# Performance work log

Measured on AMD Instinct MI355X. Metric: run time of the kernel, lower is better.

Reference implementation:

```python
import jax, jax.numpy as jnp
import numpy as np

HEADS = 16
DIM_HEAD = 64

def setup_inputs() -> dict:
    key = jax.random.key(0)
    ks = jax.random.split(key, 5)
    B, S, D = 2, 2048, 1024
    return {
        "hidden_states": jax.random.normal(ks[0], (B, S, D), dtype=jnp.float32),
        "Wq": jax.random.normal(ks[1], (D, D), dtype=jnp.float32) * (D ** -0.5),
        "Wkv": jax.random.normal(ks[2], (D, D), dtype=jnp.float32) * (D ** -0.5),
        "Wout": jax.random.normal(ks[3], (D, D), dtype=jnp.float32) * (D ** -0.5),
        "bout": jnp.zeros((D,), dtype=jnp.float32),
    }

def reference(hidden_states, Wq, Wkv, Wout, bout):
    B, S, D = hidden_states.shape
    H, Dh = HEADS, DIM_HEAD
    # projections (torch Linear: x @ W.T; here weights are stored as [in, out])
    q = hidden_states @ Wq            # [B, S, D]
    kv = hidden_states @ Wkv          # key == value share the to_kv projection
    q = q.reshape(B, S, H, Dh).transpose(0, 2, 1, 3)   # [B, H, S, Dh]
    k = kv.reshape(B, S, H, Dh).transpose(0, 2, 1, 3)
    v = k
    scale = 1.0 / np.sqrt(Dh).astype(np.float32)
    # ReLU attention: no softmax
    attn = jax.nn.relu(jnp.einsum("bhsd,bhtd->bhst", q, k) * scale)  # [B,H,S,S]
    out = jnp.einsum("bhst,bhtd->bhsd", attn, v)                     # [B,H,S,Dh]
    out = out.transpose(0, 2, 1, 3).reshape(B, S, H * Dh)
    return out @ Wout + bout
```

## Files before the change

kernel.cpp:

```cpp
#include <hip/hip_runtime.h>
#include <hip/hip_bf16.h>

#define HEADS  16
#define DIMH   64
#define NBATCH 2
#define SEQ    2048
#define DMODEL 1024
#define MROWS  (NBATCH * SEQ)

typedef __attribute__((ext_vector_type(8)))  short bf16x8;
typedef __attribute__((ext_vector_type(4)))  float f32x4;
typedef __attribute__((ext_vector_type(16))) float f32x16;
typedef __attribute__((ext_vector_type(4)))  float float4v;
typedef __attribute__((ext_vector_type(4)))  short short4v;

__device__ inline void glds16(const void* g, void* l) {
    __builtin_amdgcn_global_load_lds(
        (const __attribute__((address_space(1))) unsigned int*)g,
        (__attribute__((address_space(3))) unsigned int*)l, 16, 0, 0);
}

#define WAIT_VMCNT(N) asm volatile("s_waitcnt vmcnt(" #N ")" ::: "memory")
#define BARRIER() do { __builtin_amdgcn_s_barrier(); asm volatile("" ::: "memory"); } while (0)

__global__ void cvt_kernel(const float* __restrict__ in,
                           __hip_bfloat16* __restrict__ out, int n4) {
    int i = blockIdx.x * blockDim.x + threadIdx.x;
    if (i >= n4) return;
    float4v v = reinterpret_cast<const float4v*>(in)[i];
    union { short4v s; __hip_bfloat16 h[4]; } u;
#pragma unroll
    for (int j = 0; j < 4; ++j) u.h[j] = __float2bfloat16(v[j]);
    reinterpret_cast<short4v*>(out)[i] = u.s;
}

__global__ void tr_kernel(const float* __restrict__ W,
                          __hip_bfloat16* __restrict__ WT) {
    __shared__ float tile[32][33];
    int i = blockIdx.y * 32 + threadIdx.y;
    int o = blockIdx.x * 32 + threadIdx.x;
    tile[threadIdx.y][threadIdx.x] = W[i * DMODEL + o];
    __syncthreads();
    int oo = blockIdx.x * 32 + threadIdx.y;
    int ii = blockIdx.y * 32 + threadIdx.x;
    WT[oo * DMODEL + ii] = __float2bfloat16(tile[threadIdx.x][threadIdx.y]);
}


__launch_bounds__(512, 2)
__global__ void proj_kernel(const __hip_bfloat16* __restrict__ hsb,
                            const __hip_bfloat16* __restrict__ WqT,
                            const __hip_bfloat16* __restrict__ WkvT,
                            __hip_bfloat16* __restrict__ qb,
                            __hip_bfloat16* __restrict__ kb,
                            __hip_bfloat16* __restrict__ vtb) {
    __shared__ __align__(16) char SLDS[73728];
    char (*Alds)[8192]  = (char (*)[8192])SLDS;
    char (*Blds)[16384] = (char (*)[16384])(SLDS + 24576);
    char* CT = SLDS;

    const int tid  = threadIdx.x;
    const int wave = tid >> 6;
    const int lane = tid & 63;
    const int lr = lane & 15;
    const int lk = lane >> 4;
    const int wm = wave >> 2, wn = wave & 3;

    int bid = blockIdx.x;
    bid = (bid & 7) * 32 + (bid >> 3);
    const int xt = bid & 7;
    const int mt = bid >> 3;
    const bool is_q = xt < 4;
    const int mbase = mt * 128;
    const int nbase = (xt & 3) * 256;
    const __hip_bfloat16* __restrict__ WT = is_q ? WqT : WkvT;

    const char* __restrict__ Ab = (const char*)(hsb + (size_t)mbase * DMODEL);
    const char* __restrict__ Bb = (const char*)(WT + (size_t)nbase * DMODEL);

    auto stage = [&](int buf, int k0) {
        const size_t colb = (size_t)k0 * 2 + lk * 16;
        glds16(Ab + (size_t)(wave * 16 + lr) * (DMODEL * 2) + colb,
               &Alds[buf][wave * 1024]);
#pragma unroll
        for (int r = 0; r < 2; ++r)
            glds16(Bb + (size_t)((r * 8 + wave) * 16 + lr) * (DMODEL * 2) + colb,
                   &Blds[buf][r * 8192 + wave * 1024]);
    };

    stage(0, 0);
    stage(1, 32);

    f32x4 acc[4][4] = {};
    int c0 = 0;
    for (int t = 0; t < DMODEL / 32; ++t) {
        if (t < DMODEL / 32 - 1) WAIT_VMCNT(3); else WAIT_VMCNT(0);
        BARRIER();
        if (t + 2 < DMODEL / 32) {
            int sb = c0 + 2; if (sb >= 3) sb -= 3;
            stage(sb, (t + 2) * 32);
        }
        bf16x8 af[4], bfr[4];
#pragma unroll
        for (int i = 0; i < 4; ++i) {
            af[i]  = *reinterpret_cast<const bf16x8*>(&Alds[c0][(wm * 4 + i) * 1024 + lane * 16]);
            bfr[i] = *reinterpret_cast<const bf16x8*>(&Blds[c0][(wn * 4 + i) * 1024 + lane * 16]);
        }
#pragma unroll
        for (int i = 0; i < 4; ++i)
#pragma unroll
            for (int j = 0; j < 4; ++j)
                acc[i][j] = __builtin_amdgcn_mfma_f32_16x16x32_bf16(af[i], bfr[j], acc[i][j], 0, 0, 0);
        c0 = (c0 + 1 == 3) ? 0 : c0 + 1;
    }

    const float qscale = is_q ? 0.125f : 1.0f;
    const int b_ = mbase >> 11;
    const int s0 = mbase & (SEQ - 1);
    BARRIER();

#pragma unroll
    for (int i = 0; i < 4; ++i)
#pragma unroll
        for (int j = 0; j < 4; ++j)
#pragma unroll
            for (int r = 0; r < 4; ++r) {
                int m = wm * 64 + i * 16 + lk * 4 + r;
                int n = wn * 64 + j * 16 + lr;
                *reinterpret_cast<__hip_bfloat16*>(
                    &CT[m * 512 + ((n * 2) ^ (((m >> 2) & 7) << 4))]) =
                    __float2bfloat16(acc[i][j][r] * qscale);
            }
    BARRIER();

    __hip_bfloat16* __restrict__ dst0 = is_q ? qb : kb;
#pragma unroll
    for (int p = 0; p < 8; ++p) {
        int g = p * 64 + (tid >> 3);
        int m = g >> 2, seg = g & 3, o = tid & 7;
        int key = ((m >> 2) & 7) << 4;
        bf16x8 val = *reinterpret_cast<const bf16x8*>(
            &CT[m * 512 + ((seg * 128 + o * 16) ^ key)]);
        int h = (nbase >> 6) + seg;
        *reinterpret_cast<bf16x8*>(
            &dst0[(((size_t)b_ * HEADS + h) * SEQ + s0 + m) * DIMH + o * 8]) = val;
    }

    if (!is_q) {
        BARRIER();
#pragma unroll
        for (int i = 0; i < 4; ++i)
#pragma unroll
            for (int j = 0; j < 4; ++j)
#pragma unroll
                for (int r = 0; r < 4; ++r) {
                    int m = wm * 64 + i * 16 + lk * 4 + r;
                    int n = wn * 64 + j * 16 + lr;
                    *reinterpret_cast<__hip_bfloat16*>(
                        &CT[n * 256 + ((m * 2) ^ ((n & 7) << 4))]) =
                        __float2bfloat16(acc[i][j][r]);
                }
        BARRIER();
#pragma unroll
        for (int p = 0; p < 8; ++p) {
            int g = p * 64 + (tid >> 3);
            int n = g >> 1, half = g & 1, o = tid & 7;
            int key2 = (n & 7) << 4;
            int D = half * 64 + o * 8;
            int mm = D >> 4, H = o & 1;
            union { unsigned long long d[2]; bf16x8 v; } val;
            val.d[0] = *reinterpret_cast<const unsigned long long*>(
                &CT[n * 256 + ((mm * 32 + H * 8) ^ key2)]);
            val.d[1] = *reinterpret_cast<const unsigned long long*>(
                &CT[n * 256 + ((mm * 32 + 16 + H * 8) ^ key2)]);
            int h = (nbase >> 6) + (n >> 6);
            int dh = n & 63;
            *reinterpret_cast<bf16x8*>(
                &vtb[(((size_t)b_ * HEADS + h) * DIMH + dh) * SEQ + s0 + D]) = val.v;
        }
    }
}

__launch_bounds__(512, 2)
__global__ void outproj_kernel(const __hip_bfloat16* __restrict__ ao,
                               const __hip_bfloat16* __restrict__ WoT,
                               const float* __restrict__ bout,
                               float* __restrict__ out) {
    __shared__ __align__(16) char Alds[3][8192];
    __shared__ __align__(16) char Blds[3][8192];
    const int tid  = threadIdx.x;
    const int wave = tid >> 6;
    const int lane = tid & 63;
    const int lr = lane & 15;
    const int lk = lane >> 4;
    const int wm = wave >> 1, wn = wave & 1;

    int bid = blockIdx.x;
    bid = (bid & 7) * 32 + (bid >> 3);
    const int xt = bid & 7;
    const int mt = bid >> 3;
    const int mbase = mt * 128;
    const int nbase = xt * 128;

    const char* __restrict__ Ab = (const char*)(ao + (size_t)mbase * DMODEL);
    const char* __restrict__ Bb = (const char*)(WoT + (size_t)nbase * DMODEL);

    auto stage = [&](int buf, int k0) {
        const size_t colb = (size_t)k0 * 2 + lk * 16;
        glds16(Ab + (size_t)(wave * 16 + lr) * (DMODEL * 2) + colb,
               &Alds[buf][wave * 1024]);
        glds16(Bb + (size_t)(wave * 16 + lr) * (DMODEL * 2) + colb,
               &Blds[buf][wave * 1024]);
    };

    stage(0, 0);
    stage(1, 32);

    f32x4 acc[2][4] = {};
    int c0 = 0;
    for (int t = 0; t < DMODEL / 32; ++t) {
        if (t < DMODEL / 32 - 1) WAIT_VMCNT(2); else WAIT_VMCNT(0);
        BARRIER();
        if (t + 2 < DMODEL / 32) {
            int sb = c0 + 2; if (sb >= 3) sb -= 3;
            stage(sb, (t + 2) * 32);
        }
        bf16x8 af[2], bfr[4];
#pragma unroll
        for (int i = 0; i < 2; ++i)
            af[i] = *reinterpret_cast<const bf16x8*>(&Alds[c0][(wm * 2 + i) * 1024 + lane * 16]);
#pragma unroll
        for (int j = 0; j < 4; ++j)
            bfr[j] = *reinterpret_cast<const bf16x8*>(&Blds[c0][(wn * 4 + j) * 1024 + lane * 16]);
#pragma unroll
        for (int i = 0; i < 2; ++i)
#pragma unroll
            for (int j = 0; j < 4; ++j)
                acc[i][j] = __builtin_amdgcn_mfma_f32_16x16x32_bf16(af[i], bfr[j], acc[i][j], 0, 0, 0);
        c0 = (c0 + 1 == 3) ? 0 : c0 + 1;
    }

#pragma unroll
    for (int j = 0; j < 4; ++j) {
        const int n = nbase + wn * 64 + j * 16 + lr;
        const float bias = bout[n];
#pragma unroll
        for (int i = 0; i < 2; ++i) {
#pragma unroll
            for (int r = 0; r < 4; ++r) {
                int m = mbase + wm * 32 + i * 16 + lk * 4 + r;
                out[(size_t)m * DMODEL + n] = acc[i][j][r] + bias;
            }
        }
    }
}

__launch_bounds__(256, 2)
__global__ void attn_kernel(const __hip_bfloat16* __restrict__ qb,
                            const __hip_bfloat16* __restrict__ kb,
                            const __hip_bfloat16* __restrict__ vtb,
                            __hip_bfloat16* __restrict__ ao) {
    __shared__ __align__(16) char Klds[4][8192];
    __shared__ __align__(16) char Vlds[4][8192];
    const int lane = threadIdx.x & 63;
    const int wave = threadIdx.x >> 6;
    const int l32  = lane & 31;
    const int hi   = lane >> 5;

    int bid = blockIdx.x;
    bid = (bid & 7) * 64 + (bid >> 3);
    const int bh   = bid >> 4;
    const int qblk = bid & 15;
    const int b_ = bh >> 4, h = bh & 15;
    const int qbase = qblk * 128 + wave * 32;

    const __hip_bfloat16* __restrict__ Q = qb + (size_t)bh * SEQ * DIMH;
    const char* __restrict__ Kg = (const char*)(kb  + (size_t)bh * SEQ * DIMH);
    const char* __restrict__ Vg = (const char*)(vtb + (size_t)bh * DIMH * SEQ);

    bf16x8 qf[4];
#pragma unroll
    for (int ks = 0; ks < 4; ++ks)
        qf[ks] = *reinterpret_cast<const bf16x8*>(
            &Q[(size_t)(qbase + l32) * DIMH + ks * 16 + hi * 8]);

    auto stage = [&](int buf, int t0) {
#pragma unroll
        for (int p = 0; p < 2; ++p) {
            glds16(Kg + (size_t)(t0 + p * 32 + (lane & 31)) * 128 +
                       wave * 32 + (lane >> 5) * 16,
                   &Klds[buf][(p * 4 + wave) * 1024]);
            const int rv = p * 4 + wave;
            glds16(Vg + (size_t)((rv & 1) * 32 + (lane & 31)) * (SEQ * 2) +
                       (size_t)(t0 + (rv >> 1) * 16) * 2 + (lane >> 5) * 16,
                   &Vlds[buf][rv * 1024]);
        }
    };

    f32x16 acco[2] = {};
    f32x16 sp0, sp1;

    auto do_qk = [&](const char* Kc) {
        sp0 = f32x16{}; sp1 = f32x16{};
        __builtin_amdgcn_s_setprio(1);
#pragma unroll
        for (int ks = 0; ks < 4; ++ks) {
            bf16x8 k0f = *reinterpret_cast<const bf16x8*>(Kc + ks * 1024 + lane * 16);
            bf16x8 k1f = *reinterpret_cast<const bf16x8*>(Kc + (4 + ks) * 1024 + lane * 16);
            sp0 = __builtin_amdgcn_mfma_f32_32x32x16_bf16(k0f, qf[ks], sp0, 0, 0, 0);
            sp1 = __builtin_amdgcn_mfma_f32_32x32x16_bf16(k1f, qf[ks], sp1, 0, 0, 0);
        }
        __builtin_amdgcn_s_setprio(0);
    };

    auto do_packpv = [&](const char* Vc) {
        __builtin_amdgcn_s_setprio(1);
#pragma unroll
        for (int kt = 0; kt < 4; ++kt) {
            union { __hip_bfloat16 hh[8]; bf16x8 v; } pa;
            const int rb = (kt & 1) * 8;
#pragma unroll
            for (int j = 0; j < 8; ++j) {
                float x = (kt < 2) ? sp0[rb + j] : sp1[rb + j];
                pa.hh[j] = __float2bfloat16(fmaxf(x, 0.f));
            }
#pragma unroll
            for (int nt = 0; nt < 2; ++nt) {
                bf16x8 vbv = *reinterpret_cast<const bf16x8*>(
                    Vc + (kt * 2 + nt) * 1024 + lane * 16);
                acco[nt] = __builtin_amdgcn_mfma_f32_32x32x16_bf16(pa.v, vbv, acco[nt], 0, 0, 0);
            }
        }
        __builtin_amdgcn_s_setprio(0);
    };

    stage(0, 0);
    stage(1, 64);

    WAIT_VMCNT(4);
    BARRIER();
    stage(2, 128);
    do_qk(Klds[0]);

    for (int t = 1; t < SEQ / 64; ++t) {
        if (t < SEQ / 64 - 1) WAIT_VMCNT(4); else WAIT_VMCNT(0);
        BARRIER();
        if (t + 2 < SEQ / 64) stage((t + 2) & 3, (t + 2) * 64);
        do_packpv(Vlds[(t - 1) & 3]);
        do_qk(Klds[t & 3]);
    }
    do_packpv(Vlds[(SEQ / 64 - 1) & 3]);

#pragma unroll
    for (int nt = 0; nt < 2; ++nt) {
#pragma unroll
        for (int r = 0; r < 16; ++r) {
            int q = qbase + (r & 3) + 8 * (r >> 2) + 4 * hi;
            ao[(size_t)(b_ * SEQ + q) * DMODEL + h * 64 + nt * 32 + l32] =
                __float2bfloat16(acco[nt][r]);
        }
    }
}

extern "C" void kernel_launch(void* const* d_in, const int* in_sizes, int n_in,
                              void* d_out, int out_size, void* d_ws, size_t ws_size,
                              hipStream_t stream) {
    const float* hs   = (const float*)d_in[0];
    const float* Wq   = (const float*)d_in[1];
    const float* Wkv  = (const float*)d_in[2];
    const float* Wout = (const float*)d_in[3];
    const float* bout = (const float*)d_in[4];
    float* out = (float*)d_out;

    char* ws = (char*)d_ws;
    size_t off = 0;
    auto alloc = [&](size_t bytes) { char* p = ws + off; off += bytes; return p; };
    __hip_bfloat16* hsb  = (__hip_bfloat16*)alloc((size_t)MROWS * DMODEL * 2);
    __hip_bfloat16* WqT  = (__hip_bfloat16*)alloc((size_t)DMODEL * DMODEL * 2);
    __hip_bfloat16* WkvT = (__hip_bfloat16*)alloc((size_t)DMODEL * DMODEL * 2);
    __hip_bfloat16* WoT  = (__hip_bfloat16*)alloc((size_t)DMODEL * DMODEL * 2);
    __hip_bfloat16* qb   = (__hip_bfloat16*)alloc((size_t)MROWS * DMODEL * 2);
    __hip_bfloat16* kb   = (__hip_bfloat16*)alloc((size_t)MROWS * DMODEL * 2);
    __hip_bfloat16* vtb  = (__hip_bfloat16*)alloc((size_t)MROWS * DMODEL * 2);
    __hip_bfloat16* ao   = hsb;

    cvt_kernel<<<(MROWS * DMODEL / 4 + 255) / 256, 256, 0, stream>>>(hs, hsb, MROWS * DMODEL / 4);
    dim3 trg(32, 32), trb(32, 32);
    tr_kernel<<<trg, trb, 0, stream>>>(Wq, WqT);
    tr_kernel<<<trg, trb, 0, stream>>>(Wkv, WkvT);
    tr_kernel<<<trg, trb, 0, stream>>>(Wout, WoT);

    proj_kernel<<<256, 512, 0, stream>>>(hsb, WqT, WkvT, qb, kb, vtb);

    attn_kernel<<<NBATCH * HEADS * (SEQ / 128), 256, 0, stream>>>(qb, kb, vtb, ao);

    outproj_kernel<<<256, 512, 0, stream>>>(ao, WoT, bout, out);
}
```

Before: 120.6 us.

## Split attention over key range with 512-thread blocks and combine partials

The attention kernel now uses 512-thread blocks covering 256 queries each, and splits the key sequence into two halves handled by separate blocks. Each block writes fp32 partial outputs to a workspace, and a new combine kernel sums the two partials and converts them to bf16 for the output projection. Bigger blocks halve the K/V staging traffic per query, and the key split keeps the same block count of 512. The cost is an extra kernel launch plus writing and re-reading two fp32 partial tensors of about 16 MB each.

```diff
diff --git a/kernel.cpp b/kernel.cpp
--- a/kernel.cpp
+++ b/kernel.cpp
@@ -31,6 +31,19 @@
     union { short4v s; __hip_bfloat16 h[4]; } u;
 #pragma unroll
     for (int j = 0; j < 4; ++j) u.h[j] = __float2bfloat16(v[j]);
+    reinterpret_cast<short4v*>(out)[i] = u.s;
+}
+
+__global__ void combine_kernel(const float* __restrict__ p0,
+                               const float* __restrict__ p1,
+                               __hip_bfloat16* __restrict__ out, int n4) {
+    int i = blockIdx.x * blockDim.x + threadIdx.x;
+    if (i >= n4) return;
+    float4v a = reinterpret_cast<const float4v*>(p0)[i];
+    float4v b = reinterpret_cast<const float4v*>(p1)[i];
+    union { short4v s; __hip_bfloat16 h[4]; } u;
+#pragma unroll
+    for (int j = 0; j < 4; ++j) u.h[j] = __float2bfloat16(a[j] + b[j]);
     reinterpret_cast<short4v*>(out)[i] = u.s;
 }
 
@@ -255,11 +268,11 @@
     }
 }
 
-__launch_bounds__(256, 2)
+__launch_bounds__(512, 2)
 __global__ void attn_kernel(const __hip_bfloat16* __restrict__ qb,
                             const __hip_bfloat16* __restrict__ kb,
                             const __hip_bfloat16* __restrict__ vtb,
-                            __hip_bfloat16* __restrict__ ao) {
+                            float* __restrict__ po) {
     __shared__ __align__(16) char Klds[4][8192];
     __shared__ __align__(16) char Vlds[4][8192];
     const int lane = threadIdx.x & 63;
@@ -269,10 +282,12 @@
 
     int bid = blockIdx.x;
     bid = (bid & 7) * 64 + (bid >> 3);
+    const int ts   = bid & 1;
+    const int qblk = (bid >> 1) & 7;
     const int bh   = bid >> 4;
-    const int qblk = bid & 15;
     const int b_ = bh >> 4, h = bh & 15;
-    const int qbase = qblk * 128 + wave * 32;
+    const int qbase = qblk * 256 + wave * 32;
+    const int tbeg = ts * (SEQ / 2);
 
     const __hip_bfloat16* __restrict__ Q = qb + (size_t)bh * SEQ * DIMH;
     const char* __restrict__ Kg = (const char*)(kb  + (size_t)bh * SEQ * DIMH);
@@ -285,16 +300,12 @@
             &Q[(size_t)(qbase + l32) * DIMH + ks * 16 + hi * 8]);
 
     auto stage = [&](int buf, int t0) {
-#pragma unroll
-        for (int p = 0; p < 2; ++p) {
-            glds16(Kg + (size_t)(t0 + p * 32 + (lane & 31)) * 128 +
-                       wave * 32 + (lane >> 5) * 16,
-                   &Klds[buf][(p * 4 + wave) * 1024]);
-            const int rv = p * 4 + wave;
-            glds16(Vg + (size_t)((rv & 1) * 32 + (lane & 31)) * (SEQ * 2) +
-                       (size_t)(t0 + (rv >> 1) * 16) * 2 + (lane >> 5) * 16,
-                   &Vlds[buf][rv * 1024]);
-        }
+        glds16(Kg + (size_t)(t0 + (wave >> 2) * 32 + (lane & 31)) * 128 +
+                   (wave & 3) * 32 + (lane >> 5) * 16,
+               &Klds[buf][wave * 1024]);
+        glds16(Vg + (size_t)((wave & 1) * 32 + (lane & 31)) * (SEQ * 2) +
+                   (size_t)(t0 + (wave >> 1) * 16) * 2 + (lane >> 5) * 16,
+               &Vlds[buf][wave * 1024]);
     };
 
     f32x16 acco[2] = {};
@@ -334,30 +345,31 @@
         __builtin_amdgcn_s_setprio(0);
     };
 
-    stage(0, 0);
-    stage(1, 64);
-
-    WAIT_VMCNT(4);
+    const int NT = SEQ / 2 / 64;
+    stage(0, tbeg);
+    stage(1, tbeg + 64);
+
+    WAIT_VMCNT(2);
     BARRIER();
-    stage(2, 128);
+    stage(2, tbeg + 128);
     do_qk(Klds[0]);
 
-    for (int t = 1; t < SEQ / 64; ++t) {
-        if (t < SEQ / 64 - 1) WAIT_VMCNT(4); else WAIT_VMCNT(0);
+    for (int t = 1; t < NT; ++t) {
+        if (t < NT - 1) WAIT_VMCNT(2); else WAIT_VMCNT(0);
         BARRIER();
-        if (t + 2 < SEQ / 64) stage((t + 2) & 3, (t + 2) * 64);
+        if (t + 2 < NT) stage((t + 2) & 3, tbeg + (t + 2) * 64);
         do_packpv(Vlds[(t - 1) & 3]);
         do_qk(Klds[t & 3]);
     }
-    do_packpv(Vlds[(SEQ / 64 - 1) & 3]);
-
+    do_packpv(Vlds[(NT - 1) & 3]);
+
+    float* __restrict__ PO = po + (size_t)ts * MROWS * DMODEL;
 #pragma unroll
     for (int nt = 0; nt < 2; ++nt) {
 #pragma unroll
         for (int r = 0; r < 16; ++r) {
             int q = qbase + (r & 3) + 8 * (r >> 2) + 4 * hi;
-            ao[(size_t)(b_ * SEQ + q) * DMODEL + h * 64 + nt * 32 + l32] =
-                __float2bfloat16(acco[nt][r]);
+            PO[(size_t)(b_ * SEQ + q) * DMODEL + h * 64 + nt * 32 + l32] = acco[nt][r];
         }
     }
 }
@@ -382,6 +394,7 @@
     __hip_bfloat16* qb   = (__hip_bfloat16*)alloc((size_t)MROWS * DMODEL * 2);
     __hip_bfloat16* kb   = (__hip_bfloat16*)alloc((size_t)MROWS * DMODEL * 2);
     __hip_bfloat16* vtb  = (__hip_bfloat16*)alloc((size_t)MROWS * DMODEL * 2);
+    float*          po   = (float*)alloc((size_t)2 * MROWS * DMODEL * 4);
     __hip_bfloat16* ao   = hsb;
 
     cvt_kernel<<<(MROWS * DMODEL / 4 + 255) / 256, 256, 0, stream>>>(hs, hsb, MROWS * DMODEL / 4);
@@ -392,7 +405,10 @@
 
     proj_kernel<<<256, 512, 0, stream>>>(hsb, WqT, WkvT, qb, kb, vtb);
 
-    attn_kernel<<<NBATCH * HEADS * (SEQ / 128), 256, 0, stream>>>(qb, kb, vtb, ao);
+    attn_kernel<<<512, 512, 0, stream>>>(qb, kb, vtb, po);
+
+    combine_kernel<<<(MROWS * DMODEL / 4 + 255) / 256, 256, 0, stream>>>(
+        po, po + (size_t)MROWS * DMODEL, ao, MROWS * DMODEL / 4);
 
     outproj_kernel<<<256, 512, 0, stream>>>(ao, WoT, bout, out);
 }
```

Measured after the change: 120.9 us. About the same (+0.2%).

## Replace LDS-staged attention with single-wave blocks loading K/V directly to registers

Applied to the files above, without the earlier changes.

The attention kernel drops the shared-memory K/V ring buffer and its barriers. Each 64-thread block now handles 32 queries and loads K and V fragments straight from global memory into registers, double-buffered across two register sets. This removes LDS traffic and block-wide synchronisation, but K/V reuse across waves now depends on L2/L1 instead of shared memory, and register pressure rises.

```diff
diff --git a/kernel.cpp b/kernel.cpp
--- a/kernel.cpp
+++ b/kernel.cpp
@@ -255,24 +255,21 @@
     }
 }
 
-__launch_bounds__(256, 2)
+__launch_bounds__(64, 2)
 __global__ void attn_kernel(const __hip_bfloat16* __restrict__ qb,
                             const __hip_bfloat16* __restrict__ kb,
                             const __hip_bfloat16* __restrict__ vtb,
                             __hip_bfloat16* __restrict__ ao) {
-    __shared__ __align__(16) char Klds[4][8192];
-    __shared__ __align__(16) char Vlds[4][8192];
     const int lane = threadIdx.x & 63;
-    const int wave = threadIdx.x >> 6;
     const int l32  = lane & 31;
     const int hi   = lane >> 5;
 
     int bid = blockIdx.x;
-    bid = (bid & 7) * 64 + (bid >> 3);
-    const int bh   = bid >> 4;
-    const int qblk = bid & 15;
+    bid = (bid & 7) * 256 + (bid >> 3);
+    const int bh = bid >> 6;
+    const int qw = bid & 63;
     const int b_ = bh >> 4, h = bh & 15;
-    const int qbase = qblk * 128 + wave * 32;
+    const int qbase = qw * 32;
 
     const __hip_bfloat16* __restrict__ Q = qb + (size_t)bh * SEQ * DIMH;
     const char* __restrict__ Kg = (const char*)(kb  + (size_t)bh * SEQ * DIMH);
@@ -284,37 +281,31 @@
         qf[ks] = *reinterpret_cast<const bf16x8*>(
             &Q[(size_t)(qbase + l32) * DIMH + ks * 16 + hi * 8]);
 
-    auto stage = [&](int buf, int t0) {
-#pragma unroll
-        for (int p = 0; p < 2; ++p) {
-            glds16(Kg + (size_t)(t0 + p * 32 + (lane & 31)) * 128 +
-                       wave * 32 + (lane >> 5) * 16,
-                   &Klds[buf][(p * 4 + wave) * 1024]);
-            const int rv = p * 4 + wave;
-            glds16(Vg + (size_t)((rv & 1) * 32 + (lane & 31)) * (SEQ * 2) +
-                       (size_t)(t0 + (rv >> 1) * 16) * 2 + (lane >> 5) * 16,
-                   &Vlds[buf][rv * 1024]);
-        }
+    auto LOADKV = [&](bf16x8 (&kf)[8], bf16x8 (&vf)[8], int t0) {
+#pragma unroll
+        for (int rh = 0; rh < 2; ++rh)
+#pragma unroll
+            for (int ks = 0; ks < 4; ++ks)
+                kf[rh * 4 + ks] = *reinterpret_cast<const bf16x8*>(
+                    Kg + (size_t)(t0 + rh * 32 + l32) * 128 + ks * 32 + hi * 16);
+#pragma unroll
+        for (int kt = 0; kt < 4; ++kt)
+#pragma unroll
+            for (int nt = 0; nt < 2; ++nt)
+                vf[kt * 2 + nt] = *reinterpret_cast<const bf16x8*>(
+                    Vg + (size_t)(nt * 32 + l32) * (SEQ * 2) + (size_t)(t0 + kt * 16) * 2 + hi * 16);
     };
 
     f32x16 acco[2] = {};
-    f32x16 sp0, sp1;
-
-    auto do_qk = [&](const char* Kc) {
-        sp0 = f32x16{}; sp1 = f32x16{};
+
+    auto COMPUTE = [&](const bf16x8 (&kf)[8], const bf16x8 (&vf)[8]) {
+        f32x16 sp0 = {}, sp1 = {};
         __builtin_amdgcn_s_setprio(1);
 #pragma unroll
         for (int ks = 0; ks < 4; ++ks) {
-            bf16x8 k0f = *reinterpret_cast<const bf16x8*>(Kc + ks * 1024 + lane * 16);
-            bf16x8 k1f = *reinterpret_cast<const bf16x8*>(Kc + (4 + ks) * 1024 + lane * 16);
-            sp0 = __builtin_amdgcn_mfma_f32_32x32x16_bf16(k0f, qf[ks], sp0, 0, 0, 0);
-            sp1 = __builtin_amdgcn_mfma_f32_32x32x16_bf16(k1f, qf[ks], sp1, 0, 0, 0);
-        }
-        __builtin_amdgcn_s_setprio(0);
-    };
-
-    auto do_packpv = [&](const char* Vc) {
-        __builtin_amdgcn_s_setprio(1);
+            sp0 = __builtin_amdgcn_mfma_f32_32x32x16_bf16(kf[ks], qf[ks], sp0, 0, 0, 0);
+            sp1 = __builtin_amdgcn_mfma_f32_32x32x16_bf16(kf[4 + ks], qf[ks], sp1, 0, 0, 0);
+        }
 #pragma unroll
         for (int kt = 0; kt < 4; ++kt) {
             union { __hip_bfloat16 hh[8]; bf16x8 v; } pa;
@@ -325,31 +316,24 @@
                 pa.hh[j] = __float2bfloat16(fmaxf(x, 0.f));
             }
 #pragma unroll
-            for (int nt = 0; nt < 2; ++nt) {
-                bf16x8 vbv = *reinterpret_cast<const bf16x8*>(
-                    Vc + (kt * 2 + nt) * 1024 + lane * 16);
-                acco[nt] = __builtin_amdgcn_mfma_f32_32x32x16_bf16(pa.v, vbv, acco[nt], 0, 0, 0);
-            }
+            for (int nt = 0; nt < 2; ++nt)
+                acco[nt] = __builtin_amdgcn_mfma_f32_32x32x16_bf16(
+                    pa.v, vf[kt * 2 + nt], acco[nt], 0, 0, 0);
         }
         __builtin_amdgcn_s_setprio(0);
     };
 
-    stage(0, 0);
-    stage(1, 64);
-
-    WAIT_VMCNT(4);
-    BARRIER();
-    stage(2, 128);
-    do_qk(Klds[0]);
-
-    for (int t = 1; t < SEQ / 64; ++t) {
-        if (t < SEQ / 64 - 1) WAIT_VMCNT(4); else WAIT_VMCNT(0);
-        BARRIER();
-        if (t + 2 < SEQ / 64) stage((t + 2) & 3, (t + 2) * 64);
-        do_packpv(Vlds[(t - 1) & 3]);
-        do_qk(Klds[t & 3]);
-    }
-    do_packpv(Vlds[(SEQ / 64 - 1) & 3]);
+    bf16x8 kfA[8], vfA[8], kfB[8], vfB[8];
+    const int NT = SEQ / 64;
+
+    LOADKV(kfA, vfA, 0);
+#pragma unroll 1
+    for (int t = 0; t < NT; t += 2) {
+        LOADKV(kfB, vfB, (t + 1) * 64);
+        COMPUTE(kfA, vfA);
+        if (t + 2 < NT) LOADKV(kfA, vfA, (t + 2) * 64);
+        COMPUTE(kfB, vfB);
+    }
 
 #pragma unroll
     for (int nt = 0; nt < 2; ++nt) {
@@ -392,7 +376,7 @@
 
     proj_kernel<<<256, 512, 0, stream>>>(hsb, WqT, WkvT, qb, kb, vtb);
 
-    attn_kernel<<<NBATCH * HEADS * (SEQ / 128), 256, 0, stream>>>(qb, kb, vtb, ao);
+    attn_kernel<<<2048, 64, 0, stream>>>(qb, kb, vtb, ao);
 
     outproj_kernel<<<256, 512, 0, stream>>>(ao, WoT, bout, out);
 }
```

Measured after the change: 193.1 us. 1.6x slower.

## Retile projection to 128x128 blocks and widen attention blocks to 8 waves

Applied to the files above, without the earlier changes.

The projection GEMM tile shrinks from 128x256 to 128x128. This doubles the grid to 512 blocks, halves LDS use and raises the occupancy hint to 4. The attention kernel moves to 512-thread blocks that each cover 256 queries, so every staged K/V tile is shared by twice as many waves. Its software pipeline, which overlapped QK of one tile with PV of the previous one, is replaced by a simpler fused compute per tile. The aims are better CU fill in the projection and more K/V reuse in attention, at the cost of losing the QK/PV overlap and lowering per-wave reuse in the GEMM.

```diff
diff --git a/kernel.cpp b/kernel.cpp
--- a/kernel.cpp
+++ b/kernel.cpp
@@ -47,16 +47,16 @@
 }
 
 
-__launch_bounds__(512, 2)
+__launch_bounds__(512, 4)
 __global__ void proj_kernel(const __hip_bfloat16* __restrict__ hsb,
                             const __hip_bfloat16* __restrict__ WqT,
                             const __hip_bfloat16* __restrict__ WkvT,
                             __hip_bfloat16* __restrict__ qb,
                             __hip_bfloat16* __restrict__ kb,
                             __hip_bfloat16* __restrict__ vtb) {
-    __shared__ __align__(16) char SLDS[73728];
-    char (*Alds)[8192]  = (char (*)[8192])SLDS;
-    char (*Blds)[16384] = (char (*)[16384])(SLDS + 24576);
+    __shared__ __align__(16) char SLDS[49152];
+    char (*Alds)[8192] = (char (*)[8192])SLDS;
+    char (*Blds)[8192] = (char (*)[8192])(SLDS + 24576);
     char* CT = SLDS;
 
     const int tid  = threadIdx.x;
@@ -64,15 +64,15 @@
     const int lane = tid & 63;
     const int lr = lane & 15;
     const int lk = lane >> 4;
-    const int wm = wave >> 2, wn = wave & 3;
+    const int wm = wave >> 1, wn = wave & 1;
 
     int bid = blockIdx.x;
-    bid = (bid & 7) * 32 + (bid >> 3);
-    const int xt = bid & 7;
-    const int mt = bid >> 3;
-    const bool is_q = xt < 4;
+    bid = (bid & 7) * 64 + (bid >> 3);
+    const int xt = bid & 15;
+    const int mt = bid >> 4;
+    const bool is_q = xt < 8;
     const int mbase = mt * 128;
-    const int nbase = (xt & 3) * 256;
+    const int nbase = (xt & 7) * 128;
     const __hip_bfloat16* __restrict__ WT = is_q ? WqT : WkvT;
 
     const char* __restrict__ Ab = (const char*)(hsb + (size_t)mbase * DMODEL);
@@ -80,34 +80,32 @@
 
     auto stage = [&](int buf, int k0) {
         const size_t colb = (size_t)k0 * 2 + lk * 16;
-        glds16(Ab + (size_t)(wave * 16 + lr) * (DMODEL * 2) + colb,
-               &Alds[buf][wave * 1024]);
-#pragma unroll
-        for (int r = 0; r < 2; ++r)
-            glds16(Bb + (size_t)((r * 8 + wave) * 16 + lr) * (DMODEL * 2) + colb,
-                   &Blds[buf][r * 8192 + wave * 1024]);
+        const size_t rowoff = (size_t)(wave * 16 + lr) * (DMODEL * 2);
+        glds16(Ab + rowoff + colb, &Alds[buf][wave * 1024]);
+        glds16(Bb + rowoff + colb, &Blds[buf][wave * 1024]);
     };
 
     stage(0, 0);
     stage(1, 32);
 
-    f32x4 acc[4][4] = {};
+    f32x4 acc[2][4] = {};
     int c0 = 0;
     for (int t = 0; t < DMODEL / 32; ++t) {
-        if (t < DMODEL / 32 - 1) WAIT_VMCNT(3); else WAIT_VMCNT(0);
+        if (t < DMODEL / 32 - 1) WAIT_VMCNT(2); else WAIT_VMCNT(0);
         BARRIER();
         if (t + 2 < DMODEL / 32) {
             int sb = c0 + 2; if (sb >= 3) sb -= 3;
             stage(sb, (t + 2) * 32);
         }
-        bf16x8 af[4], bfr[4];
-#pragma unroll
-        for (int i = 0; i < 4; ++i) {
-            af[i]  = *reinterpret_cast<const bf16x8*>(&Alds[c0][(wm * 4 + i) * 1024 + lane * 16]);
-            bfr[i] = *reinterpret_cast<const bf16x8*>(&Blds[c0][(wn * 4 + i) * 1024 + lane * 16]);
-        }
-#pragma unroll
-        for (int i = 0; i < 4; ++i)
+        bf16x8 af[2], bfr[4];
+#pragma unroll
+        for (int i = 0; i < 2; ++i)
+            af[i] = *reinterpret_cast<const bf16x8*>(&Alds[c0][(wm * 2 + i) * 1024 + lane * 16]);
+#pragma unroll
+        for (int j = 0; j < 4; ++j)
+            bfr[j] = *reinterpret_cast<const bf16x8*>(&Blds[c0][(wn * 4 + j) * 1024 + lane * 16]);
+#pragma unroll
+        for (int i = 0; i < 2; ++i)
 #pragma unroll
             for (int j = 0; j < 4; ++j)
                 acc[i][j] = __builtin_amdgcn_mfma_f32_16x16x32_bf16(af[i], bfr[j], acc[i][j], 0, 0, 0);
@@ -117,44 +115,44 @@
     const float qscale = is_q ? 0.125f : 1.0f;
     const int b_ = mbase >> 11;
     const int s0 = mbase & (SEQ - 1);
+    const int h0 = nbase >> 6;
     BARRIER();
 
 #pragma unroll
-    for (int i = 0; i < 4; ++i)
+    for (int i = 0; i < 2; ++i)
 #pragma unroll
         for (int j = 0; j < 4; ++j)
 #pragma unroll
             for (int r = 0; r < 4; ++r) {
-                int m = wm * 64 + i * 16 + lk * 4 + r;
+                int m = wm * 32 + i * 16 + lk * 4 + r;
                 int n = wn * 64 + j * 16 + lr;
                 *reinterpret_cast<__hip_bfloat16*>(
-                    &CT[m * 512 + ((n * 2) ^ (((m >> 2) & 7) << 4))]) =
+                    &CT[m * 256 + ((n * 2) ^ (((m >> 2) & 7) << 4))]) =
                     __float2bfloat16(acc[i][j][r] * qscale);
             }
     BARRIER();
 
     __hip_bfloat16* __restrict__ dst0 = is_q ? qb : kb;
 #pragma unroll
-    for (int p = 0; p < 8; ++p) {
+    for (int p = 0; p < 4; ++p) {
         int g = p * 64 + (tid >> 3);
-        int m = g >> 2, seg = g & 3, o = tid & 7;
+        int m = g >> 1, hseg = g & 1, o = tid & 7;
         int key = ((m >> 2) & 7) << 4;
         bf16x8 val = *reinterpret_cast<const bf16x8*>(
-            &CT[m * 512 + ((seg * 128 + o * 16) ^ key)]);
-        int h = (nbase >> 6) + seg;
+            &CT[m * 256 + ((hseg * 128 + o * 16) ^ key)]);
         *reinterpret_cast<bf16x8*>(
-            &dst0[(((size_t)b_ * HEADS + h) * SEQ + s0 + m) * DIMH + o * 8]) = val;
+            &dst0[(((size_t)b_ * HEADS + h0 + hseg) * SEQ + s0 + m) * DIMH + o * 8]) = val;
     }
 
     if (!is_q) {
         BARRIER();
 #pragma unroll
-        for (int i = 0; i < 4; ++i)
+        for (int i = 0; i < 2; ++i)
 #pragma unroll
             for (int j = 0; j < 4; ++j)
 #pragma unroll
                 for (int r = 0; r < 4; ++r) {
-                    int m = wm * 64 + i * 16 + lk * 4 + r;
+                    int m = wm * 32 + i * 16 + lk * 4 + r;
                     int n = wn * 64 + j * 16 + lr;
                     *reinterpret_cast<__hip_bfloat16*>(
                         &CT[n * 256 + ((m * 2) ^ ((n & 7) << 4))]) =
@@ -162,7 +160,7 @@
                 }
         BARRIER();
 #pragma unroll
-        for (int p = 0; p < 8; ++p) {
+        for (int p = 0; p < 4; ++p) {
             int g = p * 64 + (tid >> 3);
             int n = g >> 1, half = g & 1, o = tid & 7;
             int key2 = (n & 7) << 4;
@@ -173,7 +171,7 @@
                 &CT[n * 256 + ((mm * 32 + H * 8) ^ key2)]);
             val.d[1] = *reinterpret_cast<const unsigned long long*>(
                 &CT[n * 256 + ((mm * 32 + 16 + H * 8) ^ key2)]);
-            int h = (nbase >> 6) + (n >> 6);
+            int h = h0 + (n >> 6);
             int dh = n & 63;
             *reinterpret_cast<bf16x8*>(
                 &vtb[(((size_t)b_ * HEADS + h) * DIMH + dh) * SEQ + s0 + D]) = val.v;
@@ -255,7 +253,7 @@
     }
 }
 
-__launch_bounds__(256, 2)
+__launch_bounds__(512, 2)
 __global__ void attn_kernel(const __hip_bfloat16* __restrict__ qb,
                             const __hip_bfloat16* __restrict__ kb,
                             const __hip_bfloat16* __restrict__ vtb,
@@ -268,11 +266,11 @@
     const int hi   = lane >> 5;
 
     int bid = blockIdx.x;
-    bid = (bid & 7) * 64 + (bid >> 3);
-    const int bh   = bid >> 4;
-    const int qblk = bid & 15;
+    bid = (bid & 7) * 32 + (bid >> 3);
+    const int qblk = bid & 7;
+    const int bh   = bid >> 3;
     const int b_ = bh >> 4, h = bh & 15;
-    const int qbase = qblk * 128 + wave * 32;
+    const int qbase = qblk * 256 + wave * 32;
 
     const __hip_bfloat16* __restrict__ Q = qb + (size_t)bh * SEQ * DIMH;
     const char* __restrict__ Kg = (const char*)(kb  + (size_t)bh * SEQ * DIMH);
@@ -285,23 +283,18 @@
             &Q[(size_t)(qbase + l32) * DIMH + ks * 16 + hi * 8]);
 
     auto stage = [&](int buf, int t0) {
-#pragma unroll
-        for (int p = 0; p < 2; ++p) {
-            glds16(Kg + (size_t)(t0 + p * 32 + (lane & 31)) * 128 +
-                       wave * 32 + (lane >> 5) * 16,
-                   &Klds[buf][(p * 4 + wave) * 1024]);
-            const int rv = p * 4 + wave;
-            glds16(Vg + (size_t)((rv & 1) * 32 + (lane & 31)) * (SEQ * 2) +
-                       (size_t)(t0 + (rv >> 1) * 16) * 2 + (lane >> 5) * 16,
-                   &Vlds[buf][rv * 1024]);
-        }
+        glds16(Kg + (size_t)(t0 + (wave >> 2) * 32 + (lane & 31)) * 128 +
+                   (wave & 3) * 32 + (lane >> 5) * 16,
+               &Klds[buf][wave * 1024]);
+        glds16(Vg + (size_t)((wave & 1) * 32 + (lane & 31)) * (SEQ * 2) +
+                   (size_t)(t0 + (wave >> 1) * 16) * 2 + (lane >> 5) * 16,
+               &Vlds[buf][wave * 1024]);
     };
 
     f32x16 acco[2] = {};
-    f32x16 sp0, sp1;
-
-    auto do_qk = [&](const char* Kc) {
-        sp0 = f32x16{}; sp1 = f32x16{};
+
+    auto compute = [&](const char* Kc, const char* Vc) {
+        f32x16 sp0 = {}, sp1 = {};
         __builtin_amdgcn_s_setprio(1);
 #pragma unroll
         for (int ks = 0; ks < 4; ++ks) {
@@ -310,11 +303,6 @@
             sp0 = __builtin_amdgcn_mfma_f32_32x32x16_bf16(k0f, qf[ks], sp0, 0, 0, 0);
             sp1 = __builtin_amdgcn_mfma_f32_32x32x16_bf16(k1f, qf[ks], sp1, 0, 0, 0);
         }
-        __builtin_amdgcn_s_setprio(0);
-    };
-
-    auto do_packpv = [&](const char* Vc) {
-        __builtin_amdgcn_s_setprio(1);
 #pragma unroll
         for (int kt = 0; kt < 4; ++kt) {
             union { __hip_bfloat16 hh[8]; bf16x8 v; } pa;
@@ -334,32 +322,25 @@
         __builtin_amdgcn_s_setprio(0);
     };
 
+    const int NT = SEQ / 64;
     stage(0, 0);
     stage(1, 64);
 
-    WAIT_VMCNT(4);
-    BARRIER();
-    stage(2, 128);
-    do_qk(Klds[0]);
-
-    for (int t = 1; t < SEQ / 64; ++t) {
-        if (t < SEQ / 64 - 1) WAIT_VMCNT(4); else WAIT_VMCNT(0);
-        BARRIER();
-        if (t + 2 < SEQ / 64) stage((t + 2) & 3, (t + 2) * 64);
-        do_packpv(Vlds[(t - 1) & 3]);
-        do_qk(Klds[t & 3]);
-    }
-    do_packpv(Vlds[(SEQ / 64 - 1) & 3]);
-
-#pragma unroll
-    for (int nt = 0; nt < 2; ++nt) {
+    for (int t = 0; t < NT; ++t) {
+        if (t < NT - 1) WAIT_VMCNT(2); else WAIT_VMCNT(0);
+        BARRIER();
+        if (t + 2 < NT) stage((t + 2) & 3, (t + 2) * 64);
+        compute(Klds[t & 3], Vlds[t & 3]);
+    }
+
+#pragma unroll
+    for (int nt = 0; nt < 2; ++nt)
 #pragma unroll
         for (int r = 0; r < 16; ++r) {
             int q = qbase + (r & 3) + 8 * (r >> 2) + 4 * hi;
             ao[(size_t)(b_ * SEQ + q) * DMODEL + h * 64 + nt * 32 + l32] =
                 __float2bfloat16(acco[nt][r]);
         }
-    }
 }
 
 extern "C" void kernel_launch(void* const* d_in, const int* in_sizes, int n_in,
@@ -390,9 +371,9 @@
     tr_kernel<<<trg, trb, 0, stream>>>(Wkv, WkvT);
     tr_kernel<<<trg, trb, 0, stream>>>(Wout, WoT);
 
-    proj_kernel<<<256, 512, 0, stream>>>(hsb, WqT, WkvT, qb, kb, vtb);
-
-    attn_kernel<<<NBATCH * HEADS * (SEQ / 128), 256, 0, stream>>>(qb, kb, vtb, ao);
+    proj_kernel<<<512, 512, 0, stream>>>(hsb, WqT, WkvT, qb, kb, vtb);
+
+    attn_kernel<<<256, 512, 0, stream>>>(qb, kb, vtb, ao);
 
     outproj_kernel<<<256, 512, 0, stream>>>(ao, WoT, bout, out);
 }
```

After: 126.5 us. +4.9%, slower.
